# Optimization experiments

Hardware: AMD Instinct MI355X
Metric: run time of the kernel (lower is better)

The kernel has to match this reference:

```python
import jax, jax.numpy as jnp
import numpy as np

LK = 8  # db4 has 8 taps
LEVEL = 5
# pywt.Wavelet('db4').filter_bank[0] == dec_lo
DB4_LO = np.array([-0.010597401784997278, 0.032883011666982945, 0.030841381835986965,
                   -0.18703481171888114, -0.02798376941698385, 0.6308807679295904,
                   0.7148465705525415, 0.23037781330885523], dtype=np.float32)
DN = ('NCH', 'OIH', 'NCH')


def _wpt_kernels(level):
    # Filter_Free WPT: distinct kernel per child node; parent j even -> (lp, hp), odd -> (hp, lp)
    cmf = (-1.0) ** np.arange(LK)
    k_lp = DB4_LO
    k_hp = (DB4_LO[::-1] * cmf).astype(np.float32)
    ks = []
    for i in range(level):
        rows = []
        for j in range(2 ** i):
            rows += [k_lp, k_hp] if j % 2 == 0 else [k_hp, k_lp]
        ks.append(jnp.asarray(np.stack(rows)))  # [2^(i+1), LK]
    return ks


def setup_inputs() -> dict:
    key = jax.random.key(0)
    kx, kb = jax.random.split(key)
    B, N = 128, 32768
    inp = {'x': jax.random.normal(kx, (B, 1, N), dtype=jnp.float32)}
    for i, K in enumerate(_wpt_kernels(LEVEL)):
        inp[f'k{i + 1}'] = K
    for i in range(LEVEL):
        kb, sub = jax.random.split(kb)
        # small positive thresholds (Act_Init=0 would make the threshold an exact identity)
        inp[f'b{i + 1}'] = 0.1 * jax.random.uniform(sub, (2 ** (i + 1),), dtype=jnp.float32)
    return inp


def _analysis(c, K, b):
    # c: [B, G, M] parents -> [B, 2G, M//2] children; one grouped 8-tap conv for the whole level
    G = c.shape[1]
    cp = jnp.pad(c, ((0, 0), (0, 0), (LK // 2 - 1, LK // 2)))
    y = jax.lax.conv_general_dilated(cp, K[:, None, :], (2,), 'VALID',
                                     feature_group_count=G, dimension_numbers=DN)
    bb = b[None, :, None]
    # symmetric sigmoid soft-threshold (Thresh_SigSym), fused elementwise
    return y * (jax.nn.sigmoid(10.0 * (y - bb)) + jax.nn.sigmoid(-10.0 * (y + bb)))


def _synthesis(y, K):
    # adjoint of the strided analysis conv (conv_transpose): [B, 2G, M] -> [B, G, 2M]
    G = y.shape[1] // 2
    M = y.shape[2]
    W = jnp.flip(K, -1).reshape(G, 2, LK)  # sum the two children of each parent
    out = jax.lax.conv_general_dilated(y, W, (1,), [(LK - 1, LK - 1)], lhs_dilation=(2,),
                                       feature_group_count=G, dimension_numbers=DN)
    pl = LK // 2 - 1  # undo analysis left pad
    return out[:, :, pl:pl + 2 * M]


def reference(x, k1, k2, k3, k4, k5, b1, b2, b3, b4, b5):
    Ks = [k1, k2, k3, k4, k5]
    bs = [b1, b2, b3, b4, b5]
    c = x  # [B, 1, N]
    for K, b in zip(Ks, bs):
        c = _analysis(c, K, b)
    for K in Ks[::-1]:
        c = _synthesis(c, K)
    return c  # [B, 1, N] reconstruction
```

## Files before the change

### kernel.cpp

```cpp
#include <hip/hip_runtime.h>

#define TPB 384

constexpr int NSEQ = 32768;
constexpr int C0   = 2048;
constexpr float SCG = 14.4269504089f;


__device__ __forceinline__ float4 ldf4(const float* p) { return *reinterpret_cast<const float4*>(p); }
__device__ __forceinline__ void   stf4(float* p, const float4 v) { *reinterpret_cast<float4*>(p) = v; }

__device__ __forceinline__ float rfl(float x) {
    return __builtin_bit_cast(float, __builtin_amdgcn_readfirstlane(__builtin_bit_cast(int, x)));
}

__device__ __forceinline__ float gated(float y, float tb) {
    float e1 = __builtin_amdgcn_exp2f(fmaf(y, -SCG, tb));
    float e2 = __builtin_amdgcn_exp2f(fmaf(y,  SCG, tb));
    return y * (__builtin_amdgcn_rcpf(1.f + e1) + __builtin_amdgcn_rcpf(1.f + e2));
}

template<int LEin, int LEout, int P, int PAIRS, int Nlev, bool EDGE, bool LAST>
__device__ __forceinline__ void analysis4(
    const float* __restrict__ in, float* __restrict__ out,
    const float* __restrict__ lp, const float* __restrict__ hp,
    const float* __restrict__ bias, int outBase)
{
    constexpr int TPC = P / 4;
    constexpr int TOT = PAIRS * TPC;
    static_assert(TOT <= TPB, "phase must be single-generation");
    const int task = threadIdx.x;
    if (task < TOT) {
        const int c  = task / TPC;
        const int i0 = (task - c * TPC) * 4;

        const float* pe = in + c * (2 * LEin) + i0;
        const float* po = pe + LEin;
        float a[8], b[8];
        reinterpret_cast<float4*>(a)[0] = ldf4(pe);
        reinterpret_cast<float4*>(a)[1] = ldf4(pe + 4);
        reinterpret_cast<float4*>(b)[0] = ldf4(po);
        reinterpret_cast<float4*>(b)[1] = ldf4(po + 4);

        const int sw     = c & 1;
        const int ch_lp  = 2 * c + sw;
        const int ch_hp  = 2 * c + 1 - sw;
        const float tb_l = bias[ch_lp];
        const float tb_h = bias[ch_hp];

        float vl[4], vh[4];
#pragma unroll
        for (int r = 0; r < 4; ++r) {
            float yl = 0.f, yh = 0.f;
#pragma unroll
            for (int u = 0; u < 4; ++u) {
                yl = fmaf(a[r + u], lp[2 * u], yl);
                yl = fmaf(b[r + u], lp[2 * u + 1], yl);
                yh = fmaf(a[r + u], hp[2 * u], yh);
                yh = fmaf(b[r + u], hp[2 * u + 1], yh);
            }
            float wl = gated(yl, tb_l);
            float wh = gated(yh, tb_h);
            if (EDGE) {
                const bool ok = ((unsigned)(outBase + i0 + r) < (unsigned)Nlev);
                wl = ok ? wl : 0.f;
                wh = ok ? wh : 0.f;
            }
            vl[r] = wl; vh[r] = wh;
        }

        if (LAST) {
            stf4(out + ch_lp * LEout + i0, make_float4(vl[0], vl[1], vl[2], vl[3]));
            stf4(out + ch_hp * LEout + i0, make_float4(vh[0], vh[1], vh[2], vh[3]));
        } else {
            const int j0 = i0 >> 1;
            float* ol = out + ch_lp * (2 * LEout);
            float* oh = out + ch_hp * (2 * LEout);
            *reinterpret_cast<float2*>(ol + j0)         = make_float2(vl[0], vl[2]);
            *reinterpret_cast<float2*>(ol + LEout + j0) = make_float2(vl[1], vl[3]);
            *reinterpret_cast<float2*>(oh + j0)         = make_float2(vh[0], vh[2]);
            *reinterpret_cast<float2*>(oh + LEout + j0) = make_float2(vh[1], vh[3]);
        }
    }
}

template<int Sin, int Sout, int G, int Nlev, bool EDGE>
__device__ __forceinline__ void synth8(
    const float* __restrict__ in, float* __restrict__ out,
    const float* __restrict__ lp, const float* __restrict__ hp, int outBase)
{
    constexpr int TPG = Sout / 8;
    constexpr int TOT = G * TPG;
    static_assert(TOT <= TPB, "phase must be single-generation");
    const int task = threadIdx.x;
    if (task < TOT) {
        const int g   = task / TPG;
        const int nl0 = (task - g * TPG) * 8;
        const int sw  = g & 1;

        float ya[8], yb[8];
        {
            const float* p0 = in + (2 * g + sw)     * Sin + nl0 / 2;
            const float* p1 = in + (2 * g + 1 - sw) * Sin + nl0 / 2;
            reinterpret_cast<float4*>(ya)[0] = ldf4(p0);
            reinterpret_cast<float4*>(ya)[1] = ldf4(p0 + 4);
            reinterpret_cast<float4*>(yb)[0] = ldf4(p1);
            reinterpret_cast<float4*>(yb)[1] = ldf4(p1 + 4);
        }

        float o[8];
#pragma unroll
        for (int r = 0; r < 8; ++r) {
            const int jr = (r + 1) >> 1;
            const int kb = 7 - (r & 1);
            float acc = 0.f;
#pragma unroll
            for (int q = 0; q < 4; ++q) {
                acc = fmaf(ya[jr + q], lp[kb - 2 * q], acc);
                acc = fmaf(yb[jr + q], hp[kb - 2 * q], acc);
            }
            if (EDGE) {
                const bool ok = ((unsigned)(outBase + nl0 + r) < (unsigned)Nlev);
                acc = ok ? acc : 0.f;
            }
            o[r] = acc;
        }
        float* op = out + g * Sout + nl0;
        stf4(op,     make_float4(o[0], o[1], o[2], o[3]));
        stf4(op + 4, make_float4(o[4], o[5], o[6], o[7]));
    }
}

template<bool EDGE>
__device__ __forceinline__ void run_chunk(
    const float* __restrict__ xb, float* __restrict__ ob, int s,
    float* __restrict__ bufA, float* __restrict__ bufB,
    const float* __restrict__ lp, const float* __restrict__ hp,
    const float* __restrict__ bss)
{
    const int tid = threadIdx.x;

    {
        const int base = s - 221;
#pragma unroll
        for (int k = 0; k < 4; ++k) {
            const int j = tid + TPB * k;
            if (j < 1276) {
                const int g0 = base + 2 * j;
                if (EDGE) {
                    bufA[j]        = ((unsigned)g0       < (unsigned)NSEQ) ? xb[g0]     : 0.f;
                    bufA[1276 + j] = ((unsigned)(g0 + 1) < (unsigned)NSEQ) ? xb[g0 + 1] : 0.f;
                } else {
                    bufA[j]        = xb[g0];
                    bufA[1276 + j] = xb[g0 + 1];
                }
            }
        }
    }
    __syncthreads();

    analysis4<1276, 636, 1272,  1, 16384, EDGE, false>(bufA, bufB, lp, hp, bss + 0,  (s >> 1) - 109);
    __syncthreads();
    analysis4< 636, 316,  632,  2,  8192, EDGE, false>(bufB, bufA, lp, hp, bss + 2,  (s >> 2) - 53);
    __syncthreads();
    analysis4< 316, 156,  312,  4,  4096, EDGE, false>(bufA, bufB, lp, hp, bss + 6,  (s >> 3) - 25);
    __syncthreads();
    analysis4< 156,  76,  152,  8,  2048, EDGE, false>(bufB, bufA, lp, hp, bss + 14, (s >> 4) - 11);
    __syncthreads();
    analysis4<  76,  72,   72, 16,  1024, EDGE, true >(bufA, bufB, lp, hp, bss + 30, (s >> 5) - 4);
    __syncthreads();

    synth8<  72,  136, 16,  2048, EDGE>(bufB, bufA, lp, hp, (s >> 4) - 4);
    __syncthreads();
    synth8< 136,  264,  8,  4096, EDGE>(bufA, bufB, lp, hp, (s >> 3) - 4);
    __syncthreads();
    synth8< 264,  520,  4,  8192, EDGE>(bufB, bufA, lp, hp, (s >> 2) - 4);
    __syncthreads();
    synth8< 520, 1032,  2, 16384, EDGE>(bufA, bufB, lp, hp, (s >> 1) - 4);
    __syncthreads();

    if (tid < 256) {
        const int i0 = tid * 8;
        float ya[12], yb[12];
        {
            const float* p0 = bufB + i0 / 2;
            const float* p1 = p0 + 1032;
            reinterpret_cast<float4*>(ya)[0] = ldf4(p0);
            reinterpret_cast<float4*>(ya)[1] = ldf4(p0 + 4);
            reinterpret_cast<float4*>(ya)[2] = ldf4(p0 + 8);
            reinterpret_cast<float4*>(yb)[0] = ldf4(p1);
            reinterpret_cast<float4*>(yb)[1] = ldf4(p1 + 4);
            reinterpret_cast<float4*>(yb)[2] = ldf4(p1 + 8);
        }
        float o[8];
#pragma unroll
        for (int r = 0; r < 8; ++r) {
            const int jr = ((r + 1) >> 1) + 2;
            const int kb = 7 - (r & 1);
            float acc = 0.f;
#pragma unroll
            for (int q = 0; q < 4; ++q) {
                acc = fmaf(ya[jr + q], lp[kb - 2 * q], acc);
                acc = fmaf(yb[jr + q], hp[kb - 2 * q], acc);
            }
            o[r] = acc;
        }
        stf4(ob + i0,     make_float4(o[0], o[1], o[2], o[3]));
        stf4(ob + i0 + 4, make_float4(o[4], o[5], o[6], o[7]));
    }
}

__global__ __launch_bounds__(TPB, 8) void wpt_fused(
    const float* __restrict__ x,
    const float* __restrict__ K1, const float* __restrict__ K2,
    const float* __restrict__ K3, const float* __restrict__ K4,
    const float* __restrict__ K5,
    const float* __restrict__ B1, const float* __restrict__ B2,
    const float* __restrict__ B3, const float* __restrict__ B4,
    const float* __restrict__ B5,
    float* __restrict__ out)
{
    __shared__ __align__(16) float bufA[2552];
    __shared__ __align__(16) float bufB[2544];
    __shared__ float bss[62];

    const int tid   = threadIdx.x;
    const int batch = blockIdx.x >> 4;
    const int cid   = blockIdx.x & 15;
    const int s     = cid * C0;

    float lp[8], hp[8];
#pragma unroll
    for (int t = 0; t < 8; ++t) {
        lp[t] = rfl(K1[t]);
        hp[t] = rfl(K1[8 + t]);
    }

    {
        const float* bin[5] = {B1, B2, B3, B4, B5};
        const int boff[5] = {0, 2, 6, 14, 30};
#pragma unroll
        for (int l = 0; l < 5; ++l)
            for (int i = tid; i < (2 << l); i += TPB) bss[boff[l] + i] = SCG * bin[l][i];
    }

    const float* xb = x + batch * NSEQ;
    float* ob = out + batch * NSEQ + s;

    if (cid == 0 || cid == 15)
        run_chunk<true >(xb, ob, s, bufA, bufB, lp, hp, bss);
    else
        run_chunk<false>(xb, ob, s, bufA, bufB, lp, hp, bss);
}

extern "C" void kernel_launch(void* const* d_in, const int* in_sizes, int n_in,
                              void* d_out, int out_size, void* d_ws, size_t ws_size,
                              hipStream_t stream) {
    const int nbatch = in_sizes[0] / NSEQ;
    wpt_fused<<<dim3(nbatch * (NSEQ / C0)), dim3(TPB), 0, stream>>>(
        (const float*)d_in[0],
        (const float*)d_in[1], (const float*)d_in[2],
        (const float*)d_in[3], (const float*)d_in[4],
        (const float*)d_in[5],
        (const float*)d_in[6], (const float*)d_in[7],
        (const float*)d_in[8], (const float*)d_in[9],
        (const float*)d_in[10],
        (float*)d_out);
}
```

Before: 119.6 us.

## Run inner wavelet levels per-wavefront in private columns to drop block barriers

Raises block size to 512 threads (8 wavefronts) and assigns each of the 8 level-3 channels to its own wavefront with a private LDS column. Analysis levels 4–5 and synthesis levels 5–4 then run inside that wavefront with no __syncthreads between them, cutting four block-wide barriers. The final output stage now writes 4 outputs per thread across all 512 threads instead of 8 per thread on 256. The inner stages use only about 33–38 of 64 lanes, and the larger block with __launch_bounds__(512,8) may limit registers or occupancy. It also relies on intra-wave LDS ordering without explicit barriers.

```diff
diff --git a/kernel.cpp b/kernel.cpp
--- a/kernel.cpp
+++ b/kernel.cpp
@@ -1,9 +1,10 @@
 #include <hip/hip_runtime.h>
 
-#define TPB 384
+#define TPB 512
 
 constexpr int NSEQ = 32768;
 constexpr int C0   = 2048;
+constexpr int COLW = 320;
 constexpr float SCG = 14.4269504089f;
 
 
@@ -20,8 +21,8 @@
     return y * (__builtin_amdgcn_rcpf(1.f + e1) + __builtin_amdgcn_rcpf(1.f + e2));
 }
 
-template<int LEin, int LEout, int P, int PAIRS, int Nlev, bool EDGE, bool LAST>
-__device__ __forceinline__ void analysis4(
+template<int LEin, int LEout, int P, int PAIRS, int Nlev, bool EDGE, int OUTSTRIDE, int EOOFF>
+__device__ __forceinline__ void analysisN(
     const float* __restrict__ in, float* __restrict__ out,
     const float* __restrict__ lp, const float* __restrict__ hp,
     const float* __restrict__ bias, int outBase)
@@ -69,23 +70,18 @@
             vl[r] = wl; vh[r] = wh;
         }
 
-        if (LAST) {
-            stf4(out + ch_lp * LEout + i0, make_float4(vl[0], vl[1], vl[2], vl[3]));
-            stf4(out + ch_hp * LEout + i0, make_float4(vh[0], vh[1], vh[2], vh[3]));
-        } else {
-            const int j0 = i0 >> 1;
-            float* ol = out + ch_lp * (2 * LEout);
-            float* oh = out + ch_hp * (2 * LEout);
-            *reinterpret_cast<float2*>(ol + j0)         = make_float2(vl[0], vl[2]);
-            *reinterpret_cast<float2*>(ol + LEout + j0) = make_float2(vl[1], vl[3]);
-            *reinterpret_cast<float2*>(oh + j0)         = make_float2(vh[0], vh[2]);
-            *reinterpret_cast<float2*>(oh + LEout + j0) = make_float2(vh[1], vh[3]);
-        }
-    }
-}
-
-template<int Sin, int Sout, int G, int Nlev, bool EDGE>
-__device__ __forceinline__ void synth8(
+        const int j0 = i0 >> 1;
+        float* ol = out + ch_lp * OUTSTRIDE;
+        float* oh = out + ch_hp * OUTSTRIDE;
+        *reinterpret_cast<float2*>(ol + j0)         = make_float2(vl[0], vl[2]);
+        *reinterpret_cast<float2*>(ol + EOOFF + j0) = make_float2(vl[1], vl[3]);
+        *reinterpret_cast<float2*>(oh + j0)         = make_float2(vh[0], vh[2]);
+        *reinterpret_cast<float2*>(oh + EOOFF + j0) = make_float2(vh[1], vh[3]);
+    }
+}
+
+template<int INSTRIDE, int Sout, int G, int Nlev, bool EDGE>
+__device__ __forceinline__ void synthN(
     const float* __restrict__ in, float* __restrict__ out,
     const float* __restrict__ lp, const float* __restrict__ hp, int outBase)
 {
@@ -100,8 +96,8 @@
 
         float ya[8], yb[8];
         {
-            const float* p0 = in + (2 * g + sw)     * Sin + nl0 / 2;
-            const float* p1 = in + (2 * g + 1 - sw) * Sin + nl0 / 2;
+            const float* p0 = in + (2 * g + sw)     * INSTRIDE + nl0 / 2;
+            const float* p1 = in + (2 * g + 1 - sw) * INSTRIDE + nl0 / 2;
             reinterpret_cast<float4*>(ya)[0] = ldf4(p0);
             reinterpret_cast<float4*>(ya)[1] = ldf4(p0 + 4);
             reinterpret_cast<float4*>(yb)[0] = ldf4(p1);
@@ -128,6 +124,158 @@
         float* op = out + g * Sout + nl0;
         stf4(op,     make_float4(o[0], o[1], o[2], o[3]));
         stf4(op + 4, make_float4(o[4], o[5], o[6], o[7]));
+    }
+}
+
+template<bool EDGE>
+__device__ __forceinline__ void stretch_wave(
+    float* __restrict__ bufA, float* __restrict__ bufB,
+    const float* __restrict__ lp, const float* __restrict__ hp,
+    const float* __restrict__ bss, int s)
+{
+    const int w    = threadIdx.x >> 6;
+    const int lane = threadIdx.x & 63;
+    float* colA = bufA + w * COLW;
+    float* colB = bufB + w * COLW;
+    const int sww = w & 1;
+
+    if (lane < 38) {
+        const int i0 = lane * 4;
+        const float* pe = colB + i0;
+        const float* po = pe + 156;
+        float a[8], b[8];
+        reinterpret_cast<float4*>(a)[0] = ldf4(pe);
+        reinterpret_cast<float4*>(a)[1] = ldf4(pe + 4);
+        reinterpret_cast<float4*>(b)[0] = ldf4(po);
+        reinterpret_cast<float4*>(b)[1] = ldf4(po + 4);
+        const float tb_l = bss[14 + 2 * w + sww];
+        const float tb_h = bss[14 + 2 * w + 1 - sww];
+        float vl[4], vh[4];
+#pragma unroll
+        for (int r = 0; r < 4; ++r) {
+            float yl = 0.f, yh = 0.f;
+#pragma unroll
+            for (int u = 0; u < 4; ++u) {
+                yl = fmaf(a[r + u], lp[2 * u], yl);
+                yl = fmaf(b[r + u], lp[2 * u + 1], yl);
+                yh = fmaf(a[r + u], hp[2 * u], yh);
+                yh = fmaf(b[r + u], hp[2 * u + 1], yh);
+            }
+            float wl = gated(yl, tb_l);
+            float wh = gated(yh, tb_h);
+            if (EDGE) {
+                const bool ok = ((unsigned)(((s >> 4) - 11) + i0 + r) < 2048u);
+                wl = ok ? wl : 0.f;
+                wh = ok ? wh : 0.f;
+            }
+            vl[r] = wl; vh[r] = wh;
+        }
+        const int j0 = i0 >> 1;
+        float* ol = colA + sww * 152;
+        float* oh = colA + (1 - sww) * 152;
+        *reinterpret_cast<float2*>(ol + j0)      = make_float2(vl[0], vl[2]);
+        *reinterpret_cast<float2*>(ol + 76 + j0) = make_float2(vl[1], vl[3]);
+        *reinterpret_cast<float2*>(oh + j0)      = make_float2(vh[0], vh[2]);
+        *reinterpret_cast<float2*>(oh + 76 + j0) = make_float2(vh[1], vh[3]);
+    }
+
+    if (lane < 36) {
+        const int l  = (lane >= 18) ? 1 : 0;
+        const int i0 = (lane - 18 * l) * 4;
+        const float* pe = colA + l * 152 + i0;
+        const float* po = pe + 76;
+        float a[8], b[8];
+        reinterpret_cast<float4*>(a)[0] = ldf4(pe);
+        reinterpret_cast<float4*>(a)[1] = ldf4(pe + 4);
+        reinterpret_cast<float4*>(b)[0] = ldf4(po);
+        reinterpret_cast<float4*>(b)[1] = ldf4(po + 4);
+        const int cg = 2 * w + l;
+        const float tb_l = bss[30 + 2 * cg + l];
+        const float tb_h = bss[30 + 2 * cg + 1 - l];
+        float vl[4], vh[4];
+#pragma unroll
+        for (int r = 0; r < 4; ++r) {
+            float yl = 0.f, yh = 0.f;
+#pragma unroll
+            for (int u = 0; u < 4; ++u) {
+                yl = fmaf(a[r + u], lp[2 * u], yl);
+                yl = fmaf(b[r + u], lp[2 * u + 1], yl);
+                yh = fmaf(a[r + u], hp[2 * u], yh);
+                yh = fmaf(b[r + u], hp[2 * u + 1], yh);
+            }
+            float wl = gated(yl, tb_l);
+            float wh = gated(yh, tb_h);
+            if (EDGE) {
+                const bool ok = ((unsigned)(((s >> 5) - 4) + i0 + r) < 1024u);
+                wl = ok ? wl : 0.f;
+                wh = ok ? wh : 0.f;
+            }
+            vl[r] = wl; vh[r] = wh;
+        }
+        stf4(colB + (3 * l) * 72 + i0, make_float4(vl[0], vl[1], vl[2], vl[3]));
+        stf4(colB + (l + 1) * 72 + i0, make_float4(vh[0], vh[1], vh[2], vh[3]));
+    }
+
+    if (lane < 34) {
+        const int gl  = (lane >= 17) ? 1 : 0;
+        const int nl0 = (lane - 17 * gl) * 8;
+        const float* p0 = colB + (3 * gl) * 72 + nl0 / 2;
+        const float* p1 = colB + (gl + 1) * 72 + nl0 / 2;
+        float ya[8], yb[8];
+        reinterpret_cast<float4*>(ya)[0] = ldf4(p0);
+        reinterpret_cast<float4*>(ya)[1] = ldf4(p0 + 4);
+        reinterpret_cast<float4*>(yb)[0] = ldf4(p1);
+        reinterpret_cast<float4*>(yb)[1] = ldf4(p1 + 4);
+        float o[8];
+#pragma unroll
+        for (int r = 0; r < 8; ++r) {
+            const int jr = (r + 1) >> 1;
+            const int kb = 7 - (r & 1);
+            float acc = 0.f;
+#pragma unroll
+            for (int q = 0; q < 4; ++q) {
+                acc = fmaf(ya[jr + q], lp[kb - 2 * q], acc);
+                acc = fmaf(yb[jr + q], hp[kb - 2 * q], acc);
+            }
+            if (EDGE) {
+                const bool ok = ((unsigned)(((s >> 4) - 4) + nl0 + r) < 2048u);
+                acc = ok ? acc : 0.f;
+            }
+            o[r] = acc;
+        }
+        float* op = colA + gl * 136 + nl0;
+        stf4(op,     make_float4(o[0], o[1], o[2], o[3]));
+        stf4(op + 4, make_float4(o[4], o[5], o[6], o[7]));
+    }
+
+    if (lane < 33) {
+        const int nl0 = lane * 8;
+        const float* p0 = colA + sww * 136 + nl0 / 2;
+        const float* p1 = colA + (1 - sww) * 136 + nl0 / 2;
+        float ya[8], yb[8];
+        reinterpret_cast<float4*>(ya)[0] = ldf4(p0);
+        reinterpret_cast<float4*>(ya)[1] = ldf4(p0 + 4);
+        reinterpret_cast<float4*>(yb)[0] = ldf4(p1);
+        reinterpret_cast<float4*>(yb)[1] = ldf4(p1 + 4);
+        float o[8];
+#pragma unroll
+        for (int r = 0; r < 8; ++r) {
+            const int jr = (r + 1) >> 1;
+            const int kb = 7 - (r & 1);
+            float acc = 0.f;
+#pragma unroll
+            for (int q = 0; q < 4; ++q) {
+                acc = fmaf(ya[jr + q], lp[kb - 2 * q], acc);
+                acc = fmaf(yb[jr + q], hp[kb - 2 * q], acc);
+            }
+            if (EDGE) {
+                const bool ok = ((unsigned)(((s >> 3) - 4) + nl0 + r) < 4096u);
+                acc = ok ? acc : 0.f;
+            }
+            o[r] = acc;
+        }
+        stf4(colB + nl0,     make_float4(o[0], o[1], o[2], o[3]));
+        stf4(colB + nl0 + 4, make_float4(o[4], o[5], o[6], o[7]));
     }
 }
 
@@ -143,7 +291,7 @@
     {
         const int base = s - 221;
 #pragma unroll
-        for (int k = 0; k < 4; ++k) {
+        for (int k = 0; k < 3; ++k) {
             const int j = tid + TPB * k;
             if (j < 1276) {
                 const int g0 = base + 2 * j;
@@ -159,42 +307,33 @@
     }
     __syncthreads();
 
-    analysis4<1276, 636, 1272,  1, 16384, EDGE, false>(bufA, bufB, lp, hp, bss + 0,  (s >> 1) - 109);
-    __syncthreads();
-    analysis4< 636, 316,  632,  2,  8192, EDGE, false>(bufB, bufA, lp, hp, bss + 2,  (s >> 2) - 53);
-    __syncthreads();
-    analysis4< 316, 156,  312,  4,  4096, EDGE, false>(bufA, bufB, lp, hp, bss + 6,  (s >> 3) - 25);
-    __syncthreads();
-    analysis4< 156,  76,  152,  8,  2048, EDGE, false>(bufB, bufA, lp, hp, bss + 14, (s >> 4) - 11);
-    __syncthreads();
-    analysis4<  76,  72,   72, 16,  1024, EDGE, true >(bufA, bufB, lp, hp, bss + 30, (s >> 5) - 4);
-    __syncthreads();
-
-    synth8<  72,  136, 16,  2048, EDGE>(bufB, bufA, lp, hp, (s >> 4) - 4);
-    __syncthreads();
-    synth8< 136,  264,  8,  4096, EDGE>(bufA, bufB, lp, hp, (s >> 3) - 4);
-    __syncthreads();
-    synth8< 264,  520,  4,  8192, EDGE>(bufB, bufA, lp, hp, (s >> 2) - 4);
-    __syncthreads();
-    synth8< 520, 1032,  2, 16384, EDGE>(bufA, bufB, lp, hp, (s >> 1) - 4);
-    __syncthreads();
-
-    if (tid < 256) {
-        const int i0 = tid * 8;
-        float ya[12], yb[12];
-        {
-            const float* p0 = bufB + i0 / 2;
-            const float* p1 = p0 + 1032;
-            reinterpret_cast<float4*>(ya)[0] = ldf4(p0);
-            reinterpret_cast<float4*>(ya)[1] = ldf4(p0 + 4);
-            reinterpret_cast<float4*>(ya)[2] = ldf4(p0 + 8);
-            reinterpret_cast<float4*>(yb)[0] = ldf4(p1);
-            reinterpret_cast<float4*>(yb)[1] = ldf4(p1 + 4);
-            reinterpret_cast<float4*>(yb)[2] = ldf4(p1 + 8);
-        }
-        float o[8];
-#pragma unroll
-        for (int r = 0; r < 8; ++r) {
+    analysisN<1276, 636, 1272, 1, 16384, EDGE, 1272, 636>(bufA, bufB, lp, hp, bss + 0, (s >> 1) - 109);
+    __syncthreads();
+    analysisN< 636, 316,  632, 2,  8192, EDGE,  632, 316>(bufB, bufA, lp, hp, bss + 2, (s >> 2) - 53);
+    __syncthreads();
+    analysisN< 316, 156,  312, 4,  4096, EDGE, COLW, 156>(bufA, bufB, lp, hp, bss + 6, (s >> 3) - 25);
+    __syncthreads();
+
+    stretch_wave<EDGE>(bufA, bufB, lp, hp, bss, s);
+    __syncthreads();
+
+    synthN<COLW,  520, 4,  8192, EDGE>(bufB, bufA, lp, hp, (s >> 2) - 4);
+    __syncthreads();
+    synthN< 520, 1032, 2, 16384, EDGE>(bufA, bufB, lp, hp, (s >> 1) - 4);
+    __syncthreads();
+
+    {
+        const int i0 = tid * 4;
+        const float* p0 = bufB + i0 / 2;
+        const float* p1 = p0 + 1032;
+        float ya[8], yb[8];
+        reinterpret_cast<float4*>(ya)[0] = ldf4(p0);
+        reinterpret_cast<float4*>(ya)[1] = ldf4(p0 + 4);
+        reinterpret_cast<float4*>(yb)[0] = ldf4(p1);
+        reinterpret_cast<float4*>(yb)[1] = ldf4(p1 + 4);
+        float o[4];
+#pragma unroll
+        for (int r = 0; r < 4; ++r) {
             const int jr = ((r + 1) >> 1) + 2;
             const int kb = 7 - (r & 1);
             float acc = 0.f;
@@ -205,8 +344,7 @@
             }
             o[r] = acc;
         }
-        stf4(ob + i0,     make_float4(o[0], o[1], o[2], o[3]));
-        stf4(ob + i0 + 4, make_float4(o[4], o[5], o[6], o[7]));
+        stf4(ob + i0, make_float4(o[0], o[1], o[2], o[3]));
     }
 }
 
@@ -220,8 +358,8 @@
     const float* __restrict__ B5,
     float* __restrict__ out)
 {
-    __shared__ __align__(16) float bufA[2552];
-    __shared__ __align__(16) float bufB[2544];
+    __shared__ __align__(16) float bufA[2560];
+    __shared__ __align__(16) float bufB[2560];
     __shared__ float bss[62];
 
     const int tid   = threadIdx.x;
```

Measured after the change: 116.1 us. 3.0% less time.
